# Kernel optimization log

Measured on AMD Instinct MI355X. Metric: run time of the kernel, lower is better.

The kernel has to match this reference:

```python
import jax, jax.numpy as jnp
import numpy as np

DIM = 1024
HEADS = 8
EV = DIM  # dim*expand - dim with expand=2
P = 2.0   # power-softmax exponent
EPS = 1e-5


def setup_inputs() -> dict:
    key = jax.random.key(0)
    k1, k2, k3 = jax.random.split(key, 3)
    B, L = 4, 2048
    x = jax.random.normal(k1, (B, L, DIM), dtype=jnp.float32)
    gamma = jnp.ones((DIM,), dtype=jnp.float32)
    beta = jnp.zeros((DIM,), dtype=jnp.float32)
    # torch nn.Linear weights are [out_features, in_features]
    w_qkv = jax.random.normal(k2, (5 * DIM, DIM), dtype=jnp.float32) * (DIM ** -0.5)
    w_out = jax.random.normal(k3, (DIM, 2 * DIM), dtype=jnp.float32) * ((2 * DIM) ** -0.5)
    return {"x": x, "gamma": gamma, "beta": beta, "w_qkv": w_qkv, "w_out": w_out}


def _layernorm(x, gamma, beta):
    xf = x.astype(jnp.float32)
    mu = jnp.mean(xf, axis=-1, keepdims=True)
    var = jnp.mean(jnp.square(xf - mu), axis=-1, keepdims=True)
    return ((xf - mu) * jax.lax.rsqrt(var + EPS)) * gamma + beta


def _p_softmax(scores, scale, p):
    # scores: [B,H,L,L] with -inf on masked entries
    s = scores.astype(jnp.float32) * scale
    if p == 1.0:
        return jax.nn.softmax(s, axis=-1)
    lse = jax.nn.logsumexp(s * p, axis=-1, keepdims=True) / p
    return jnp.exp(s - lse)


def _attention(q, k, v, heads, p):
    B, L, D = q.shape
    hd = D // heads
    q = q.reshape(B, L, heads, hd).transpose(0, 2, 1, 3)  # bhld
    k = k.reshape(B, L, heads, hd).transpose(0, 2, 1, 3)
    v = v.reshape(B, L, heads, hd).transpose(0, 2, 1, 3)
    scores = jnp.einsum('bhqd,bhkd->bhqk', q, k)
    mask = jnp.tril(jnp.ones((L, L), dtype=bool))
    scores = jnp.where(mask, scores, -jnp.inf)
    probs = _p_softmax(scores, hd ** -0.5, p).astype(q.dtype)
    out = jnp.einsum('bhqk,bhkd->bhqd', probs, v)
    return out.transpose(0, 2, 1, 3).reshape(B, L, D)


def reference(x, gamma, beta, w_qkv, w_out):
    h = _layernorm(x, gamma, beta).astype(x.dtype)
    proj = h @ w_qkv.T  # [B,L,5*DIM]
    q, k, v, lin, pre = jnp.split(proj, np.cumsum([DIM, DIM, DIM, EV]), axis=-1)
    attn = _attention(q, k, v, HEADS, P)
    branch = jnp.concatenate([lin * jax.nn.gelu(pre, approximate=False), attn], axis=-1)
    return x + branch @ w_out.T
```

## Files before the change

### kernel.cpp

```cpp
#include <hip/hip_runtime.h>
#include <hip/hip_bf16.h>
#include <math.h>

#define DIMD 1024
#define LSEQ 2048
#define BATCH 4
#define NHEAD 8
#define HD 128
#define NROWS (BATCH*LSEQ)
#define PROJC (5*DIMD)
#define BRC (2*DIMD)

typedef __attribute__((ext_vector_type(8))) short short8;
typedef __attribute__((ext_vector_type(4))) short short4v;
typedef __attribute__((ext_vector_type(4))) float floatx4;

__device__ __forceinline__ float bf2f(short s) {
  unsigned int u = ((unsigned int)(unsigned short)s) << 16;
  return __builtin_bit_cast(float, u);
}
__device__ __forceinline__ short f2bf(float f) {
  unsigned int u = __builtin_bit_cast(unsigned int, f);
  unsigned int lsb = (u >> 16) & 1u;
  u += 0x7fffu + lsb;
  return (short)(u >> 16);
}

__device__ __forceinline__ void gl2lds16(const short* g, short* l) {
  __builtin_amdgcn_global_load_lds(
      (const __attribute__((address_space(1))) unsigned int*)(unsigned long long)g,
      (__attribute__((address_space(3))) unsigned int*)(unsigned int)(unsigned long long)l,
      16, 0, 0);
}

__global__ __launch_bounds__(256) void cvt2_kernel(const float* __restrict__ s1,
    short* __restrict__ d1, int n1_4, const float* __restrict__ s2,
    short* __restrict__ d2, int n2_4) {
  int i = blockIdx.x * 256 + threadIdx.x;
  const float* src; short* dst;
  if (i < n1_4) { src = s1; dst = d1; }
  else { i -= n1_4; if (i >= n2_4) return; src = s2; dst = d2; }
  float4 v = *(const float4*)(src + (size_t)i * 4);
  short4v o;
  o[0] = f2bf(v.x); o[1] = f2bf(v.y); o[2] = f2bf(v.z); o[3] = f2bf(v.w);
  *(short4v*)(dst + (size_t)i * 4) = o;
}

__global__ __launch_bounds__(256) void ln_kernel(const float* __restrict__ x,
    const float* __restrict__ gamma, const float* __restrict__ beta,
    short* __restrict__ h) {
  int row = blockIdx.x;
  int c = threadIdx.x * 4;
  const float* xr = x + (size_t)row * DIMD;
  float4 v = *(const float4*)(xr + c);
  float f[4] = {v.x, v.y, v.z, v.w};
  float sum = 0.f, sq = 0.f;
  for (int i = 0; i < 4; ++i) { sum += f[i]; sq += f[i]*f[i]; }
  for (int off = 1; off < 64; off <<= 1) {
    sum += __shfl_xor(sum, off);
    sq  += __shfl_xor(sq, off);
  }
  __shared__ float red[8];
  int wid = threadIdx.x >> 6;
  if ((threadIdx.x & 63) == 0) { red[wid*2] = sum; red[wid*2+1] = sq; }
  __syncthreads();
  sum = red[0]+red[2]+red[4]+red[6];
  sq  = red[1]+red[3]+red[5]+red[7];
  float mu = sum * (1.0f/DIMD);
  float var = sq * (1.0f/DIMD) - mu*mu;
  float rstd = rsqrtf(var + 1e-5f);
  float4 g = *(const float4*)(gamma + c);
  float4 bb = *(const float4*)(beta + c);
  float gg[4] = {g.x, g.y, g.z, g.w};
  float bv[4] = {bb.x, bb.y, bb.z, bb.w};
  short4v o;
  for (int i = 0; i < 4; ++i)
    o[i] = f2bf((f[i] - mu) * rstd * gg[i] + bv[i]);
  *(short4v*)(h + (size_t)row * DIMD + c) = o;
}

template<int MODE>
__global__ __launch_bounds__(256) void gemm_bt(const short* __restrict__ A,
    const short* __restrict__ W, const float* __restrict__ X,
    void* __restrict__ Cv, int M, int N, int K) {
  __shared__ __align__(16) short As[128*64];
  __shared__ __align__(16) short Ws[128*64];
  int tid = threadIdx.x;
  int row0 = blockIdx.y * 128;
  int col0 = blockIdx.x * 128;
  int lane = tid & 63, wv = tid >> 6;
  int wr = (wv >> 1) * 64, wc = (wv & 1) * 64;
  int quad = lane >> 4, l16 = lane & 15;
  floatx4 acc[4][4] = {};
  int srow = lane >> 3;
  int gq = ((lane & 7) - srow) & 7;
  const short* Ag = A + (size_t)(row0 + wv*8 + srow) * K + gq*8;
  const short* Wg = W + (size_t)(col0 + wv*8 + srow) * K + gq*8;
  short* Al = As + wv*8*64;
  short* Wl = Ws + wv*8*64;
  int qsr0 = (((quad)     + (l16 & 7)) & 7) * 8;
  int qsr1 = (((quad + 4) + (l16 & 7)) & 7) * 8;
  for (int k0 = 0; k0 < K; k0 += 64) {
    __syncthreads();
    for (int c = 0; c < 4; ++c) {
      gl2lds16(Ag + k0 + (size_t)(c*32)*K, Al + c*32*64);
      gl2lds16(Wg + k0 + (size_t)(c*32)*K, Wl + c*32*64);
    }
    __syncthreads();
    short8 af[4], wf[4];
    for (int i = 0; i < 4; ++i) af[i] = *(const short8*)&As[(wr + i*16 + l16)*64 + qsr0];
    for (int j = 0; j < 4; ++j) wf[j] = *(const short8*)&Ws[(wc + j*16 + l16)*64 + qsr0];
    for (int i = 0; i < 4; ++i)
      for (int j = 0; j < 4; ++j)
        acc[i][j] = __builtin_amdgcn_mfma_f32_16x16x32_bf16(af[i], wf[j], acc[i][j], 0, 0, 0);
    for (int i = 0; i < 4; ++i) af[i] = *(const short8*)&As[(wr + i*16 + l16)*64 + qsr1];
    for (int j = 0; j < 4; ++j) wf[j] = *(const short8*)&Ws[(wc + j*16 + l16)*64 + qsr1];
    for (int i = 0; i < 4; ++i)
      for (int j = 0; j < 4; ++j)
        acc[i][j] = __builtin_amdgcn_mfma_f32_16x16x32_bf16(af[i], wf[j], acc[i][j], 0, 0, 0);
  }
  for (int i = 0; i < 4; ++i) {
    int r0 = row0 + wr + i*16 + quad*4;
    for (int j = 0; j < 4; ++j) {
      int cc = col0 + wc + j*16 + l16;
      for (int r = 0; r < 4; ++r) {
        float v = acc[i][j][r];
        size_t idx = (size_t)(r0 + r) * N + cc;
        if (MODE == 0) {
          ((short*)Cv)[idx] = f2bf(v);
        } else {
          ((float*)Cv)[idx] = v + X[idx];
        }
      }
    }
  }
}

__global__ __launch_bounds__(256) void gelu_kernel(const short* __restrict__ proj,
    short* __restrict__ branch) {
  int row = blockIdx.x;
  int c = threadIdx.x * 4;
  const short* pr = proj + (size_t)row * PROJC;
  short4v lin = *(const short4v*)(pr + 3*DIMD + c);
  short4v pre = *(const short4v*)(pr + 4*DIMD + c);
  short4v o;
  for (int i = 0; i < 4; ++i) {
    float xx = bf2f(pre[i]);
    float g = 0.5f * xx * (1.f + erff(xx * 0.70710678118654752f));
    o[i] = f2bf(bf2f(lin[i]) * g);
  }
  *(short4v*)(branch + (size_t)row * BRC + c) = o;
}

__global__ __launch_bounds__(256) void vt_kernel(const short* __restrict__ proj,
    short* __restrict__ vt) {
  int bh = blockIdx.y;
  int b = bh >> 3, hh = bh & 7;
  int l0 = blockIdx.x * 64;
  __shared__ short Ls[64][136];
  int tid = threadIdx.x;
  int r = tid >> 4, c = (tid & 15) * 8;
  const short* Vp = proj + (size_t)b * LSEQ * PROJC + 2*DIMD + hh*HD;
  for (int p = 0; p < 4; ++p)
    *(short8*)&Ls[r + p*16][c] = *(const short8*)(Vp + (size_t)(l0 + r + p*16) * PROJC + c);
  __syncthreads();
  int d = tid >> 1, lh = (tid & 1) * 32;
  short* outp = vt + ((size_t)bh * HD + d) * LSEQ + l0 + lh;
  for (int g = 0; g < 4; ++g) {
    short8 o;
    for (int j = 0; j < 8; ++j) o[j] = Ls[lh + g*8 + j][d];
    *(short8*)(outp + g*8) = o;
  }
}

__global__ __launch_bounds__(512) void attn_kernel(const short* __restrict__ proj,
    const short* __restrict__ vt, short* __restrict__ branch) {
  int bh = blockIdx.x & 31;
  int bid = blockIdx.x >> 5;
  int b = bh >> 3, hh = bh & 7;
  int tid = threadIdx.x;
  int wv = tid >> 6, lane = tid & 63, quad = lane >> 4, l16 = lane & 15;
  int qsel = (wv < 4) ? bid : (31 - bid);
  int qw = qsel * 64 + (wv & 3) * 16;

  const short* Qp  = proj + (size_t)b * LSEQ * PROJC + hh*HD;
  const short* Kp  = Qp + DIMD;
  const short* VTp = vt + (size_t)bh * HD * LSEQ;

  __shared__ short Ks[64][136];
  __shared__ short Vs[128][76];
  __shared__ short Ps[8][16][44];

  short8 qf[4];
  {
    const short* qrow = Qp + (size_t)(qw + l16) * PROJC;
    for (int s = 0; s < 4; ++s) qf[s] = *(const short8*)(qrow + s*32 + quad*8);
  }
  float lsum[4] = {0.f, 0.f, 0.f, 0.f};
  floatx4 O[8] = {};

  const float scale = 0.08838834764831845f;
  int NT = 32 - bid;
  int krow = tid >> 4;
  int kcol = (tid & 15) * 8;
  int vd = tid >> 2;
  int vk = (tid & 3) * 8;
  for (int kt = 0; kt < NT; ++kt) {
    int kb64 = kt * 64;
    short8 kv0 = *(const short8*)(Kp + (size_t)(kb64 + krow) * PROJC + kcol);
    short8 kv1 = *(const short8*)(Kp + (size_t)(kb64 + 32 + krow) * PROJC + kcol);
    short8 vv0 = *(const short8*)(VTp + (size_t)vd * LSEQ + kb64 + vk);
    short8 vv1 = *(const short8*)(VTp + (size_t)vd * LSEQ + kb64 + 32 + vk);
    __syncthreads();
    *(short8*)&Ks[krow][kcol]      = kv0;
    *(short8*)&Ks[krow + 32][kcol] = kv1;
    *(short8*)&Vs[vd][vk]          = vv0;
    *(short8*)&Vs[vd][32 + vk]     = vv1;
    __syncthreads();
    for (int hf = 0; hf < 2; ++hf) {
      int kb = kb64 + hf*32;
      if (kb <= qw + 15) {
        floatx4 s0 = {0.f,0.f,0.f,0.f}, s1 = {0.f,0.f,0.f,0.f};
        for (int s = 0; s < 4; ++s) {
          short8 kf0 = *(const short8*)&Ks[hf*32 + l16][s*32 + quad*8];
          short8 kf1 = *(const short8*)&Ks[hf*32 + 16 + l16][s*32 + quad*8];
          s0 = __builtin_amdgcn_mfma_f32_16x16x32_bf16(qf[s], kf0, s0, 0, 0, 0);
          s1 = __builtin_amdgcn_mfma_f32_16x16x32_bf16(qf[s], kf1, s1, 0, 0, 0);
        }
        int c0 = kb + l16, c1 = kb + 16 + l16;
        for (int r = 0; r < 4; ++r) {
          int q = qw + quad*4 + r;
          float w0 = (c0 <= q) ? __expf(s0[r] * scale) : 0.f;
          float w1 = (c1 <= q) ? __expf(s1[r] * scale) : 0.f;
          lsum[r] += w0*w0 + w1*w1;
          Ps[wv][quad*4+r][l16]      = f2bf(w0);
          Ps[wv][quad*4+r][16 + l16] = f2bf(w1);
        }
        asm volatile("s_waitcnt lgkmcnt(0)" ::: "memory");
        short8 pf = *(const short8*)&Ps[wv][l16][quad*8];
        for (int t8 = 0; t8 < 8; ++t8) {
          short8 vf = *(const short8*)&Vs[t8*16 + l16][hf*32 + quad*8];
          O[t8] = __builtin_amdgcn_mfma_f32_16x16x32_bf16(pf, vf, O[t8], 0, 0, 0);
        }
      }
    }
  }
  for (int r = 0; r < 4; ++r) {
    float l = lsum[r];
    for (int off = 1; off < 16; off <<= 1) l += __shfl_xor(l, off);
    float inv = rsqrtf(l);
    int q = qw + quad*4 + r;
    short* orow = branch + ((size_t)(b*LSEQ + q)) * BRC + DIMD + hh*HD;
    for (int t8 = 0; t8 < 8; ++t8)
      orow[t8*16 + l16] = f2bf(O[t8][r] * inv);
  }
}

extern "C" void kernel_launch(void* const* d_in, const int* in_sizes, int n_in,
                              void* d_out, int out_size, void* d_ws, size_t ws_size,
                              hipStream_t stream) {
  const float* x     = (const float*)d_in[0];
  const float* gamma = (const float*)d_in[1];
  const float* beta  = (const float*)d_in[2];
  const float* w_qkv = (const float*)d_in[3];
  const float* w_out = (const float*)d_in[4];
  float* out = (float*)d_out;

  char* ws = (char*)d_ws;
  short* h      = (short*)ws;
  short* proj   = (short*)(ws + (size_t)16*1024*1024);
  short* branch = (short*)(ws + (size_t)96*1024*1024);
  short* wq     = (short*)(ws + (size_t)128*1024*1024);
  short* wo     = (short*)(ws + (size_t)138*1024*1024);
  short* vt     = h;

  int n1 = PROJC*DIMD/4, n2 = DIMD*BRC/4;
  cvt2_kernel<<<(n1 + n2 + 255)/256, 256, 0, stream>>>(w_qkv, wq, n1, w_out, wo, n2);
  ln_kernel<<<NROWS, 256, 0, stream>>>(x, gamma, beta, h);
  gemm_bt<0><<<dim3(PROJC/128, NROWS/128), 256, 0, stream>>>(h, wq, nullptr, proj,
                                                             NROWS, PROJC, DIMD);
  gelu_kernel<<<NROWS, 256, 0, stream>>>(proj, branch);
  vt_kernel<<<dim3(LSEQ/64, BATCH*NHEAD), 256, 0, stream>>>(proj, vt);
  attn_kernel<<<dim3(512), 512, 0, stream>>>(proj, vt, branch);
  gemm_bt<1><<<dim3(DIMD/128, NROWS/128), 256, 0, stream>>>(branch, wo, x, out,
                                                            NROWS, DIMD, BRC);
}
```

Before: 362.7 us.

## Process two query tiles per wave in attention to reuse K/V tiles

Each wave in the attention kernel now handles two 16-row query tiles 64 rows apart, so every K/V tile staged in LDS serves 128 query rows per block instead of 64. The grid is halved to 256 blocks, with the causal pairing reworked around 128-row chunks (bid and 15-bid) to keep the work per block balanced. This cuts global K/V loads and barrier-synchronised staging per query row. In exchange, each thread holds twice the accumulator and Q-fragment registers, and there are fewer resident waves per CU to hide latency.

```diff
diff --git a/kernel.cpp b/kernel.cpp
--- a/kernel.cpp
+++ b/kernel.cpp
@@ -180,8 +180,9 @@
   int b = bh >> 3, hh = bh & 7;
   int tid = threadIdx.x;
   int wv = tid >> 6, lane = tid & 63, quad = lane >> 4, l16 = lane & 15;
-  int qsel = (wv < 4) ? bid : (31 - bid);
-  int qw = qsel * 64 + (wv & 3) * 16;
+  int qch = (wv < 4) ? bid : (15 - bid);
+  int qw0 = qch * 128 + (wv & 3) * 16;
+  int qw1 = qw0 + 64;
 
   const short* Qp  = proj + (size_t)b * LSEQ * PROJC + hh*HD;
   const short* Kp  = Qp + DIMD;
@@ -191,16 +192,20 @@
   __shared__ short Vs[128][76];
   __shared__ short Ps[8][16][44];
 
-  short8 qf[4];
+  short8 qf0[4], qf1[4];
   {
-    const short* qrow = Qp + (size_t)(qw + l16) * PROJC;
-    for (int s = 0; s < 4; ++s) qf[s] = *(const short8*)(qrow + s*32 + quad*8);
-  }
-  float lsum[4] = {0.f, 0.f, 0.f, 0.f};
-  floatx4 O[8] = {};
+    const short* qr0 = Qp + (size_t)(qw0 + l16) * PROJC;
+    const short* qr1 = Qp + (size_t)(qw1 + l16) * PROJC;
+    for (int s = 0; s < 4; ++s) {
+      qf0[s] = *(const short8*)(qr0 + s*32 + quad*8);
+      qf1[s] = *(const short8*)(qr1 + s*32 + quad*8);
+    }
+  }
+  float lsum0[4] = {0.f,0.f,0.f,0.f}, lsum1[4] = {0.f,0.f,0.f,0.f};
+  floatx4 O0[8] = {}, O1[8] = {};
 
   const float scale = 0.08838834764831845f;
-  int NT = 32 - bid;
+  int NT = 32 - 2*bid;
   int krow = tid >> 4;
   int kcol = (tid & 15) * 8;
   int vd = tid >> 2;
@@ -219,20 +224,41 @@
     __syncthreads();
     for (int hf = 0; hf < 2; ++hf) {
       int kb = kb64 + hf*32;
-      if (kb <= qw + 15) {
-        floatx4 s0 = {0.f,0.f,0.f,0.f}, s1 = {0.f,0.f,0.f,0.f};
+      if (kb <= qw1 + 15) {
+        bool doA = (kb <= qw0 + 15);
+        floatx4 sa0 = {}, sa1 = {}, sb0 = {}, sb1 = {};
         for (int s = 0; s < 4; ++s) {
           short8 kf0 = *(const short8*)&Ks[hf*32 + l16][s*32 + quad*8];
           short8 kf1 = *(const short8*)&Ks[hf*32 + 16 + l16][s*32 + quad*8];
-          s0 = __builtin_amdgcn_mfma_f32_16x16x32_bf16(qf[s], kf0, s0, 0, 0, 0);
-          s1 = __builtin_amdgcn_mfma_f32_16x16x32_bf16(qf[s], kf1, s1, 0, 0, 0);
+          if (doA) {
+            sa0 = __builtin_amdgcn_mfma_f32_16x16x32_bf16(qf0[s], kf0, sa0, 0, 0, 0);
+            sa1 = __builtin_amdgcn_mfma_f32_16x16x32_bf16(qf0[s], kf1, sa1, 0, 0, 0);
+          }
+          sb0 = __builtin_amdgcn_mfma_f32_16x16x32_bf16(qf1[s], kf0, sb0, 0, 0, 0);
+          sb1 = __builtin_amdgcn_mfma_f32_16x16x32_bf16(qf1[s], kf1, sb1, 0, 0, 0);
         }
         int c0 = kb + l16, c1 = kb + 16 + l16;
+        if (doA) {
+          for (int r = 0; r < 4; ++r) {
+            int q = qw0 + quad*4 + r;
+            float w0 = (c0 <= q) ? __expf(sa0[r] * scale) : 0.f;
+            float w1 = (c1 <= q) ? __expf(sa1[r] * scale) : 0.f;
+            lsum0[r] += w0*w0 + w1*w1;
+            Ps[wv][quad*4+r][l16]      = f2bf(w0);
+            Ps[wv][quad*4+r][16 + l16] = f2bf(w1);
+          }
+          asm volatile("s_waitcnt lgkmcnt(0)" ::: "memory");
+          short8 pf = *(const short8*)&Ps[wv][l16][quad*8];
+          for (int t8 = 0; t8 < 8; ++t8) {
+            short8 vf = *(const short8*)&Vs[t8*16 + l16][hf*32 + quad*8];
+            O0[t8] = __builtin_amdgcn_mfma_f32_16x16x32_bf16(pf, vf, O0[t8], 0, 0, 0);
+          }
+        }
         for (int r = 0; r < 4; ++r) {
-          int q = qw + quad*4 + r;
-          float w0 = (c0 <= q) ? __expf(s0[r] * scale) : 0.f;
-          float w1 = (c1 <= q) ? __expf(s1[r] * scale) : 0.f;
-          lsum[r] += w0*w0 + w1*w1;
+          int q = qw1 + quad*4 + r;
+          float w0 = (c0 <= q) ? __expf(sb0[r] * scale) : 0.f;
+          float w1 = (c1 <= q) ? __expf(sb1[r] * scale) : 0.f;
+          lsum1[r] += w0*w0 + w1*w1;
           Ps[wv][quad*4+r][l16]      = f2bf(w0);
           Ps[wv][quad*4+r][16 + l16] = f2bf(w1);
         }
@@ -240,19 +266,25 @@
         short8 pf = *(const short8*)&Ps[wv][l16][quad*8];
         for (int t8 = 0; t8 < 8; ++t8) {
           short8 vf = *(const short8*)&Vs[t8*16 + l16][hf*32 + quad*8];
-          O[t8] = __builtin_amdgcn_mfma_f32_16x16x32_bf16(pf, vf, O[t8], 0, 0, 0);
+          O1[t8] = __builtin_amdgcn_mfma_f32_16x16x32_bf16(pf, vf, O1[t8], 0, 0, 0);
         }
       }
     }
   }
   for (int r = 0; r < 4; ++r) {
-    float l = lsum[r];
-    for (int off = 1; off < 16; off <<= 1) l += __shfl_xor(l, off);
-    float inv = rsqrtf(l);
-    int q = qw + quad*4 + r;
-    short* orow = branch + ((size_t)(b*LSEQ + q)) * BRC + DIMD + hh*HD;
-    for (int t8 = 0; t8 < 8; ++t8)
-      orow[t8*16 + l16] = f2bf(O[t8][r] * inv);
+    float l0 = lsum0[r], l1 = lsum1[r];
+    for (int off = 1; off < 16; off <<= 1) {
+      l0 += __shfl_xor(l0, off);
+      l1 += __shfl_xor(l1, off);
+    }
+    float inv0 = rsqrtf(l0), inv1 = rsqrtf(l1);
+    int q0 = qw0 + quad*4 + r, q1 = qw1 + quad*4 + r;
+    short* orow0 = branch + ((size_t)(b*LSEQ + q0)) * BRC + DIMD + hh*HD;
+    short* orow1 = branch + ((size_t)(b*LSEQ + q1)) * BRC + DIMD + hh*HD;
+    for (int t8 = 0; t8 < 8; ++t8) {
+      orow0[t8*16 + l16] = f2bf(O0[t8][r] * inv0);
+      orow1[t8*16 + l16] = f2bf(O1[t8][r] * inv1);
+    }
   }
 }
 
@@ -281,7 +313,7 @@
                                                              NROWS, PROJC, DIMD);
   gelu_kernel<<<NROWS, 256, 0, stream>>>(proj, branch);
   vt_kernel<<<dim3(LSEQ/64, BATCH*NHEAD), 256, 0, stream>>>(proj, vt);
-  attn_kernel<<<dim3(512), 512, 0, stream>>>(proj, vt, branch);
+  attn_kernel<<<dim3(256), 512, 0, stream>>>(proj, vt, branch);
   gemm_bt<1><<<dim3(DIMD/128, NROWS/128), 256, 0, stream>>>(branch, wo, x, out,
                                                             NROWS, DIMD, BRC);
 }
```

After: 366.3 us. No clear change (+1.0%).
